# Kernel tuning notes

Hardware: AMD Instinct MI355X
Metric: run time of the kernel (lower is better)

The kernel has to match this reference:

```python
import jax, jax.numpy as jnp
import numpy as np

# FP4 E2M1 lookup: low 3 bits -> magnitude {0,.5,1,1.5,2,3,4,6}, bit 3 -> sign
FP4_LUT = jnp.array([0.0, 0.5, 1.0, 1.5, 2.0, 3.0, 4.0, 6.0,
                     -0.0, -0.5, -1.0, -1.5, -2.0, -3.0, -4.0, -6.0], dtype=jnp.float32)


def _dequant(packed_i32, scales, group_size):
    """packed_i32: [K/8, N] (8 FP4 nibbles per word along K); scales: [K/group_size, N] fp16.
    Returns dense [K, N] float32 weight."""
    p = packed_i32.astype(jnp.uint32)
    shifts = (jnp.arange(8, dtype=jnp.uint32) * jnp.uint32(4))
    nib = ((p[:, None, :] >> shifts[None, :, None]) & jnp.uint32(0xF)).astype(jnp.int32)  # [K/8,8,N]
    K = p.shape[0] * 8
    vals = FP4_LUT[nib.reshape(K, p.shape[1])]  # [K, N] f32
    g = jnp.arange(K) // group_size
    return vals * scales.astype(jnp.float32)[g]


def setup_inputs() -> dict:
    key = jax.random.key(0)
    k1, k2, k3, k4, k5 = jax.random.split(key, 5)
    B, H, I, G = 32, 4096, 2048, 128
    x = (jax.random.normal(k1, (B, H), dtype=jnp.float32) * 0.5).astype(jnp.float16)
    gate_up_packed = jax.random.bits(k2, (H // 8, 2 * I), dtype=jnp.uint32).astype(jnp.int32)
    down_packed = jax.random.bits(k3, (I // 8, H), dtype=jnp.uint32).astype(jnp.int32)
    gate_up_scales = (jax.random.uniform(k4, (H // G, 2 * I), minval=0.005, maxval=0.02)).astype(jnp.float16)
    down_scales = (jax.random.uniform(k5, (I // G, H), minval=0.005, maxval=0.02)).astype(jnp.float16)
    return {"x": x, "gate_up_packed": gate_up_packed, "gate_up_scales": gate_up_scales,
            "down_packed": down_packed, "down_scales": down_scales, "group_size": G}


def reference(x, gate_up_packed, gate_up_scales, down_packed, down_scales, group_size):
    w_gu = _dequant(gate_up_packed, gate_up_scales, group_size)   # [H, 2I]
    h = jnp.einsum('bh,hn->bn', x.astype(jnp.float32), w_gu)      # [B, 2I]
    inter = h.shape[1] // 2
    act = jax.nn.silu(h[:, :inter]) * h[:, inter:]                # SwiGLU
    w_d = _dequant(down_packed, down_scales, group_size)          # [I, H]
    out = jnp.einsum('bi,ih->bh', act, w_d)
    return out.astype(jnp.float16)
```

## Files before the change

### kernel.cpp

```cpp
#include <hip/hip_runtime.h>
#include <cstdint>

typedef float f32x4 __attribute__((ext_vector_type(4)));

constexpr int Bv = 32;
constexpr int Hv = 4096;
constexpr int Iv = 2048;
constexpr int N1 = 4096;

__device__ __forceinline__ long dec8(uint32_t w) {
  uint32_t lo = w & 0x07070707u;
  uint32_t hi = (w >> 4) & 0x07070707u;
  uint32_t me = __builtin_amdgcn_perm(0x4C484440u, 0x3C383000u, lo);
  uint32_t mo = __builtin_amdgcn_perm(0x4C484440u, 0x3C383000u, hi);
  uint32_t e  = me | ((w & 0x08080808u) << 4);
  uint32_t o  = mo | (w & 0x80808080u);
  uint32_t d0 = __builtin_amdgcn_perm(o, e, 0x05010400u);
  uint32_t d1 = __builtin_amdgcn_perm(o, e, 0x07030602u);
  return (long)(((uint64_t)d1 << 32) | d0);
}

__device__ __forceinline__ void quant8(const float* p, long& hi, long& lo) {
  f32x4 a = *(const f32x4*)p;
  f32x4 b = *(const f32x4*)(p + 4);
  uint32_t h0 = 0, h1 = 0;
  h0 = __builtin_amdgcn_cvt_pk_fp8_f32(a[0], a[1], h0, false);
  h0 = __builtin_amdgcn_cvt_pk_fp8_f32(a[2], a[3], h0, true);
  h1 = __builtin_amdgcn_cvt_pk_fp8_f32(b[0], b[1], h1, false);
  h1 = __builtin_amdgcn_cvt_pk_fp8_f32(b[2], b[3], h1, true);
  float r0 = a[0] - __builtin_amdgcn_cvt_f32_fp8(h0, 0);
  float r1 = a[1] - __builtin_amdgcn_cvt_f32_fp8(h0, 1);
  float r2 = a[2] - __builtin_amdgcn_cvt_f32_fp8(h0, 2);
  float r3 = a[3] - __builtin_amdgcn_cvt_f32_fp8(h0, 3);
  float r4 = b[0] - __builtin_amdgcn_cvt_f32_fp8(h1, 0);
  float r5 = b[1] - __builtin_amdgcn_cvt_f32_fp8(h1, 1);
  float r6 = b[2] - __builtin_amdgcn_cvt_f32_fp8(h1, 2);
  float r7 = b[3] - __builtin_amdgcn_cvt_f32_fp8(h1, 3);
  uint32_t l0 = 0, l1 = 0;
  l0 = __builtin_amdgcn_cvt_pk_fp8_f32(r0, r1, l0, false);
  l0 = __builtin_amdgcn_cvt_pk_fp8_f32(r2, r3, l0, true);
  l1 = __builtin_amdgcn_cvt_pk_fp8_f32(r4, r5, l1, false);
  l1 = __builtin_amdgcn_cvt_pk_fp8_f32(r6, r7, l1, true);
  hi = (long)(((uint64_t)h1 << 32) | h0);
  lo = (long)(((uint64_t)l1 << 32) | l0);
}

__global__ __launch_bounds__(1024, 4) void k_gateup(
    const float* __restrict__ x, const uint32_t* __restrict__ wp,
    const float* __restrict__ sc, float* __restrict__ hp) {
  __shared__ float lds[16 * 1024];
  const int nt = blockIdx.x >> 1;
  const int kh = blockIdx.x & 1;
  const int wid = threadIdx.x >> 6, lane = threadIdx.x & 63;
  const int q = lane >> 4, r = lane & 15;
  const int n0 = nt * 32;
  const int nA = n0 + r, nB = n0 + 16 + r;

  const int koff = kh * 2048 + wid * 128 + q * 8;
  const float* px0 = x + r * Hv + koff;
  const float* px1 = x + (r + 16) * Hv + koff;
  const uint32_t* pbA = wp + (size_t)(kh * 256 + wid * 16 + q) * N1 + nA;
  const uint32_t* pbB = pbA + 16;

  f32x4 t00 = {0,0,0,0}, t01 = {0,0,0,0}, t10 = {0,0,0,0}, t11 = {0,0,0,0};
  #pragma unroll
  for (int st = 0; st < 4; ++st) {
    long A0h, A0l, A1h, A1l;
    quant8(px0 + st * 32, A0h, A0l);
    quant8(px1 + st * 32, A1h, A1l);
    long BA = dec8(pbA[(size_t)st * 4 * N1]);
    long BB = dec8(pbB[(size_t)st * 4 * N1]);
    t00 = __builtin_amdgcn_mfma_f32_16x16x32_fp8_fp8(A0h, BA, t00, 0, 0, 0);
    t00 = __builtin_amdgcn_mfma_f32_16x16x32_fp8_fp8(A0l, BA, t00, 0, 0, 0);
    t01 = __builtin_amdgcn_mfma_f32_16x16x32_fp8_fp8(A0h, BB, t01, 0, 0, 0);
    t01 = __builtin_amdgcn_mfma_f32_16x16x32_fp8_fp8(A0l, BB, t01, 0, 0, 0);
    t10 = __builtin_amdgcn_mfma_f32_16x16x32_fp8_fp8(A1h, BA, t10, 0, 0, 0);
    t10 = __builtin_amdgcn_mfma_f32_16x16x32_fp8_fp8(A1l, BA, t10, 0, 0, 0);
    t11 = __builtin_amdgcn_mfma_f32_16x16x32_fp8_fp8(A1h, BB, t11, 0, 0, 0);
    t11 = __builtin_amdgcn_mfma_f32_16x16x32_fp8_fp8(A1l, BB, t11, 0, 0, 0);
  }
  const int g = kh * 16 + wid;
  const float sA = sc[g * N1 + nA];
  const float sB = sc[g * N1 + nB];
  float* my = lds + wid * 1024;
  #pragma unroll
  for (int j = 0; j < 4; ++j) {
    const int rw = q * 4 + j;
    my[rw * 32 + r]             = sA * t00[j];
    my[rw * 32 + 16 + r]        = sB * t01[j];
    my[(16 + rw) * 32 + r]      = sA * t10[j];
    my[(16 + rw) * 32 + 16 + r] = sB * t11[j];
  }
  __syncthreads();
  const int i = threadIdx.x;
  float sum = 0.f;
  #pragma unroll
  for (int w = 0; w < 16; ++w) sum += lds[w * 1024 + i];
  hp[(size_t)kh * (Bv * N1) + (i >> 5) * N1 + n0 + (i & 31)] = sum;
}

__global__ __launch_bounds__(256) void k_swiglu(const float* __restrict__ hp,
                                                uint32_t* __restrict__ ah,
                                                uint32_t* __restrict__ al) {
  const int t = blockIdx.x * 256 + threadIdx.x;
  const int m = t >> 9;
  const int c = (t & 511) * 4;
  constexpr int P = Bv * N1;
  const float* pg = hp + m * N1 + c;
  const float* pu = pg + Iv;
  f32x4 g = *(const f32x4*)pg + *(const f32x4*)(pg + P);
  f32x4 u = *(const f32x4*)pu + *(const f32x4*)(pu + P);
  float a[4];
  #pragma unroll
  for (int j = 0; j < 4; ++j) {
    float gv = g[j];
    float av = gv / (1.0f + __expf(-gv)) * u[j];
    a[j] = fminf(fmaxf(av, -440.0f), 440.0f);
  }
  uint32_t h = 0;
  h = __builtin_amdgcn_cvt_pk_fp8_f32(a[0], a[1], h, false);
  h = __builtin_amdgcn_cvt_pk_fp8_f32(a[2], a[3], h, true);
  float r0 = a[0] - __builtin_amdgcn_cvt_f32_fp8(h, 0);
  float r1 = a[1] - __builtin_amdgcn_cvt_f32_fp8(h, 1);
  float r2 = a[2] - __builtin_amdgcn_cvt_f32_fp8(h, 2);
  float r3 = a[3] - __builtin_amdgcn_cvt_f32_fp8(h, 3);
  uint32_t l = 0;
  l = __builtin_amdgcn_cvt_pk_fp8_f32(r0, r1, l, false);
  l = __builtin_amdgcn_cvt_pk_fp8_f32(r2, r3, l, true);
  ah[t] = h; al[t] = l;
}

__global__ __launch_bounds__(1024, 4) void k_down(
    const uint8_t* __restrict__ ah8, const uint8_t* __restrict__ al8,
    const uint32_t* __restrict__ wp, const float* __restrict__ sc,
    float* __restrict__ out) {
  __shared__ float lds[16 * 512];
  const int n0 = blockIdx.x * 16;
  const int wid = threadIdx.x >> 6, lane = threadIdx.x & 63;
  const int q = lane >> 4, r = lane & 15;
  const int n = n0 + r;

  const int koff = wid * 128 + q * 8;
  const uint8_t* pa0h = ah8 + r * Iv + koff;
  const uint8_t* pa0l = al8 + r * Iv + koff;
  const uint8_t* pa1h = ah8 + (r + 16) * Iv + koff;
  const uint8_t* pa1l = al8 + (r + 16) * Iv + koff;
  const uint32_t* pb = wp + (size_t)(wid * 16 + q) * Hv + n;

  f32x4 t0 = {0,0,0,0}, t1 = {0,0,0,0};
  #pragma unroll
  for (int st = 0; st < 4; ++st) {
    long A0h = *(const long*)(pa0h + st * 32);
    long A0l = *(const long*)(pa0l + st * 32);
    long A1h = *(const long*)(pa1h + st * 32);
    long A1l = *(const long*)(pa1l + st * 32);
    long Bf = dec8(pb[(size_t)st * 4 * Hv]);
    t0 = __builtin_amdgcn_mfma_f32_16x16x32_fp8_fp8(A0h, Bf, t0, 0, 0, 0);
    t0 = __builtin_amdgcn_mfma_f32_16x16x32_fp8_fp8(A0l, Bf, t0, 0, 0, 0);
    t1 = __builtin_amdgcn_mfma_f32_16x16x32_fp8_fp8(A1h, Bf, t1, 0, 0, 0);
    t1 = __builtin_amdgcn_mfma_f32_16x16x32_fp8_fp8(A1l, Bf, t1, 0, 0, 0);
  }
  const float sv = sc[wid * Hv + n];
  float* my = lds + wid * 512;
  #pragma unroll
  for (int j = 0; j < 4; ++j) {
    const int rw = q * 4 + j;
    my[rw * 16 + r]        = sv * t0[j];
    my[(16 + rw) * 16 + r] = sv * t1[j];
  }
  __syncthreads();
  const int i = threadIdx.x;
  if (i < 512) {
    float sum = 0.f;
    #pragma unroll
    for (int w = 0; w < 16; ++w) sum += lds[w * 512 + i];
    out[(i >> 4) * N1 + n0 + (i & 15)] = sum;
  }
}

extern "C" void kernel_launch(void* const* d_in, const int* in_sizes, int n_in,
                              void* d_out, int out_size, void* d_ws, size_t ws_size,
                              hipStream_t stream) {
  const float*    x   = (const float*)d_in[0];
  const uint32_t* gup = (const uint32_t*)d_in[1];
  const float*    gus = (const float*)d_in[2];
  const uint32_t* dnp = (const uint32_t*)d_in[3];
  const float*    dns = (const float*)d_in[4];

  float*   hp  = (float*)d_ws;
  uint8_t* a8h = (uint8_t*)d_ws + 2*(size_t)Bv*N1*sizeof(float);
  uint8_t* a8l = a8h + Bv*Iv;

  k_gateup<<<256, 1024, 0, stream>>>(x, gup, gus, hp);
  k_swiglu<<< 64,  256, 0, stream>>>(hp, (uint32_t*)a8h, (uint32_t*)a8l);
  k_down  <<<256, 1024, 0, stream>>>(a8h, a8l, dnp, dns, (float*)d_out);
}
```

Before: 90.65 us.

## Fuse SwiGLU into gate/up kernel by pairing gate and up columns per block

Each gate/up block now computes 8 gate columns and the matching 8 up columns over the full K range instead of splitting K in half. This lets it apply SwiGLU and the fp8 hi/lo quantization in-block and write the activations directly. The separate SwiGLU kernel and the fp32 partial-sum workspace round trip go away, saving one launch and global traffic. In exchange each wave handles 256 K elements with two scale groups, and the 16-column tiles give half-sector weight loads (8 gate plus 8 up columns in separate rows).

```diff
diff --git a/kernel.cpp b/kernel.cpp
--- a/kernel.cpp
+++ b/kernel.cpp
@@ -45,89 +45,73 @@
   lo = (long)(((uint64_t)l1 << 32) | l0);
 }
 
-__global__ __launch_bounds__(1024, 4) void k_gateup(
+__global__ __launch_bounds__(1024, 4) void k_gu(
     const float* __restrict__ x, const uint32_t* __restrict__ wp,
-    const float* __restrict__ sc, float* __restrict__ hp) {
-  __shared__ float lds[16 * 1024];
-  const int nt = blockIdx.x >> 1;
-  const int kh = blockIdx.x & 1;
+    const float* __restrict__ sc, uint8_t* __restrict__ a8h,
+    uint8_t* __restrict__ a8l) {
+  __shared__ float lds[16 * 512];
+  const int c0 = blockIdx.x * 8;
   const int wid = threadIdx.x >> 6, lane = threadIdx.x & 63;
   const int q = lane >> 4, r = lane & 15;
-  const int n0 = nt * 32;
-  const int nA = n0 + r, nB = n0 + 16 + r;
+  const int ncol = (r < 8) ? (c0 + r) : (Iv + c0 + (r - 8));
 
-  const int koff = kh * 2048 + wid * 128 + q * 8;
+  const int koff = wid * 256 + q * 8;
   const float* px0 = x + r * Hv + koff;
   const float* px1 = x + (r + 16) * Hv + koff;
-  const uint32_t* pbA = wp + (size_t)(kh * 256 + wid * 16 + q) * N1 + nA;
-  const uint32_t* pbB = pbA + 16;
+  const uint32_t* pb = wp + (size_t)(wid * 32 + q) * N1 + ncol;
 
-  f32x4 t00 = {0,0,0,0}, t01 = {0,0,0,0}, t10 = {0,0,0,0}, t11 = {0,0,0,0};
+  f32x4 acc0 = {0,0,0,0}, acc1 = {0,0,0,0};
   #pragma unroll
-  for (int st = 0; st < 4; ++st) {
-    long A0h, A0l, A1h, A1l;
-    quant8(px0 + st * 32, A0h, A0l);
-    quant8(px1 + st * 32, A1h, A1l);
-    long BA = dec8(pbA[(size_t)st * 4 * N1]);
-    long BB = dec8(pbB[(size_t)st * 4 * N1]);
-    t00 = __builtin_amdgcn_mfma_f32_16x16x32_fp8_fp8(A0h, BA, t00, 0, 0, 0);
-    t00 = __builtin_amdgcn_mfma_f32_16x16x32_fp8_fp8(A0l, BA, t00, 0, 0, 0);
-    t01 = __builtin_amdgcn_mfma_f32_16x16x32_fp8_fp8(A0h, BB, t01, 0, 0, 0);
-    t01 = __builtin_amdgcn_mfma_f32_16x16x32_fp8_fp8(A0l, BB, t01, 0, 0, 0);
-    t10 = __builtin_amdgcn_mfma_f32_16x16x32_fp8_fp8(A1h, BA, t10, 0, 0, 0);
-    t10 = __builtin_amdgcn_mfma_f32_16x16x32_fp8_fp8(A1l, BA, t10, 0, 0, 0);
-    t11 = __builtin_amdgcn_mfma_f32_16x16x32_fp8_fp8(A1h, BB, t11, 0, 0, 0);
-    t11 = __builtin_amdgcn_mfma_f32_16x16x32_fp8_fp8(A1l, BB, t11, 0, 0, 0);
+  for (int g = 0; g < 2; ++g) {
+    f32x4 t0 = {0,0,0,0}, t1 = {0,0,0,0};
+    #pragma unroll
+    for (int st = 0; st < 4; ++st) {
+      const int ke = g * 128 + st * 32;
+      long A0h, A0l, A1h, A1l;
+      quant8(px0 + ke, A0h, A0l);
+      quant8(px1 + ke, A1h, A1l);
+      long B = dec8(pb[(size_t)(g * 16 + st * 4) * N1]);
+      t0 = __builtin_amdgcn_mfma_f32_16x16x32_fp8_fp8(A0h, B, t0, 0, 0, 0);
+      t0 = __builtin_amdgcn_mfma_f32_16x16x32_fp8_fp8(A0l, B, t0, 0, 0, 0);
+      t1 = __builtin_amdgcn_mfma_f32_16x16x32_fp8_fp8(A1h, B, t1, 0, 0, 0);
+      t1 = __builtin_amdgcn_mfma_f32_16x16x32_fp8_fp8(A1l, B, t1, 0, 0, 0);
+    }
+    const float s = sc[(wid * 2 + g) * N1 + ncol];
+    #pragma unroll
+    for (int j = 0; j < 4; ++j) {
+      acc0[j] = fmaf(s, t0[j], acc0[j]);
+      acc1[j] = fmaf(s, t1[j], acc1[j]);
+    }
   }
-  const int g = kh * 16 + wid;
-  const float sA = sc[g * N1 + nA];
-  const float sB = sc[g * N1 + nB];
-  float* my = lds + wid * 1024;
+  float* my = lds + wid * 512;
   #pragma unroll
   for (int j = 0; j < 4; ++j) {
     const int rw = q * 4 + j;
-    my[rw * 32 + r]             = sA * t00[j];
-    my[rw * 32 + 16 + r]        = sB * t01[j];
-    my[(16 + rw) * 32 + r]      = sA * t10[j];
-    my[(16 + rw) * 32 + 16 + r] = sB * t11[j];
+    my[rw * 16 + r]        = acc0[j];
+    my[(16 + rw) * 16 + r] = acc1[j];
   }
   __syncthreads();
   const int i = threadIdx.x;
-  float sum = 0.f;
-  #pragma unroll
-  for (int w = 0; w < 16; ++w) sum += lds[w * 1024 + i];
-  hp[(size_t)kh * (Bv * N1) + (i >> 5) * N1 + n0 + (i & 31)] = sum;
-}
-
-__global__ __launch_bounds__(256) void k_swiglu(const float* __restrict__ hp,
-                                                uint32_t* __restrict__ ah,
-                                                uint32_t* __restrict__ al) {
-  const int t = blockIdx.x * 256 + threadIdx.x;
-  const int m = t >> 9;
-  const int c = (t & 511) * 4;
-  constexpr int P = Bv * N1;
-  const float* pg = hp + m * N1 + c;
-  const float* pu = pg + Iv;
-  f32x4 g = *(const f32x4*)pg + *(const f32x4*)(pg + P);
-  f32x4 u = *(const f32x4*)pu + *(const f32x4*)(pu + P);
-  float a[4];
-  #pragma unroll
-  for (int j = 0; j < 4; ++j) {
-    float gv = g[j];
-    float av = gv / (1.0f + __expf(-gv)) * u[j];
-    a[j] = fminf(fmaxf(av, -440.0f), 440.0f);
+  if (i < 512) {
+    float sum = 0.f;
+    #pragma unroll
+    for (int w = 0; w < 16; ++w) sum += lds[w * 512 + i];
+    lds[i] = sum;
   }
-  uint32_t h = 0;
-  h = __builtin_amdgcn_cvt_pk_fp8_f32(a[0], a[1], h, false);
-  h = __builtin_amdgcn_cvt_pk_fp8_f32(a[2], a[3], h, true);
-  float r0 = a[0] - __builtin_amdgcn_cvt_f32_fp8(h, 0);
-  float r1 = a[1] - __builtin_amdgcn_cvt_f32_fp8(h, 1);
-  float r2 = a[2] - __builtin_amdgcn_cvt_f32_fp8(h, 2);
-  float r3 = a[3] - __builtin_amdgcn_cvt_f32_fp8(h, 3);
-  uint32_t l = 0;
-  l = __builtin_amdgcn_cvt_pk_fp8_f32(r0, r1, l, false);
-  l = __builtin_amdgcn_cvt_pk_fp8_f32(r2, r3, l, true);
-  ah[t] = h; al[t] = l;
+  __syncthreads();
+  if (i < 256) {
+    const int row = i >> 3, c = i & 7;
+    const float gv = lds[row * 16 + c];
+    const float uv = lds[row * 16 + 8 + c];
+    float av = gv / (1.0f + __expf(-gv)) * uv;
+    av = fminf(fmaxf(av, -440.0f), 440.0f);
+    uint32_t hb = __builtin_amdgcn_cvt_pk_fp8_f32(av, av, 0, false);
+    float rv = av - __builtin_amdgcn_cvt_f32_fp8(hb, 0);
+    uint32_t lb = __builtin_amdgcn_cvt_pk_fp8_f32(rv, rv, 0, false);
+    const int off = row * Iv + c0 + c;
+    a8h[off] = (uint8_t)(hb & 0xFF);
+    a8l[off] = (uint8_t)(lb & 0xFF);
+  }
 }
 
 __global__ __launch_bounds__(1024, 4) void k_down(
@@ -187,11 +171,9 @@
   const uint32_t* dnp = (const uint32_t*)d_in[3];
   const float*    dns = (const float*)d_in[4];
 
-  float*   hp  = (float*)d_ws;
-  uint8_t* a8h = (uint8_t*)d_ws + 2*(size_t)Bv*N1*sizeof(float);
+  uint8_t* a8h = (uint8_t*)d_ws;
   uint8_t* a8l = a8h + Bv*Iv;
 
-  k_gateup<<<256, 1024, 0, stream>>>(x, gup, gus, hp);
-  k_swiglu<<< 64,  256, 0, stream>>>(hp, (uint32_t*)a8h, (uint32_t*)a8l);
-  k_down  <<<256, 1024, 0, stream>>>(a8h, a8l, dnp, dns, (float*)d_out);
+  k_gu  <<<256, 1024, 0, stream>>>(x, gup, gus, a8h, a8l);
+  k_down<<<256, 1024, 0, stream>>>(a8h, a8l, dnp, dns, (float*)d_out);
 }
```

Measured after the change: 95.45 us. 1.05x slower.
